# Optimization experiments

Measured on AMD Instinct MI355X. Metric: run time of the kernel, lower is better.

The kernel has to match this reference:

```python
import jax, jax.numpy as jnp
import numpy as np

B, N, F_IN, H, D = 2, 3000, 64, 4, 32
NEG = -1e9  # mask value used by the original layer

def setup_inputs() -> dict:
    key = jax.random.key(0)
    ks = jax.random.split(key, 6)
    h = jax.random.normal(ks[0], (B, N, F_IN), dtype=jnp.float32)
    # dense 0/1 adjacency
    a = jax.random.randint(ks[1], (B, N, N), 0, 2).astype(jnp.float32)
    kernel = jax.random.normal(ks[2], (H, F_IN, D), dtype=jnp.float32) * 0.1
    att_k1 = jax.random.normal(ks[3], (H, D), dtype=jnp.float32) * 0.1
    att_k2 = jax.random.normal(ks[4], (H, D), dtype=jnp.float32) * 0.1
    bias = jax.random.normal(ks[5], (H, D), dtype=jnp.float32) * 0.1
    return {"h": h, "a": a, "kernel": kernel, "att_k1": att_k1, "att_k2": att_k2, "bias": bias}

def reference(h, a, kernel, att_k1, att_k2, bias):
    # per-head projection: [B,H,N,D]
    feat = jnp.einsum('bnf,hfd->bhnd', h, kernel)
    e1 = jnp.einsum('bhnd,hd->bhn', feat, att_k1)  # attention (query part)
    e2 = jnp.einsum('bhnd,hd->bhn', feat, att_k2)  # attention_2 (key part)
    # dense branch: att = a * (e1_i + e2_j); NO LeakyReLU in dense path (faithful)
    adj = a[:, None]                                   # [B,1,N,N]
    scores = adj * (e1[..., :, None] + e2[..., None, :])
    scores = scores + jnp.where(adj == 0, jnp.float32(NEG), jnp.float32(0))
    att = jax.nn.softmax(scores, axis=-1)
    att = att * (adj != 0).astype(att.dtype)
    # dropout is identity at inference
    out = jnp.einsum('bhnm,bhmd->bhnd', att, feat)
    out = out + bias[None, :, None, :]
    out = jax.nn.relu(out)
    # zero out all-zero input nodes
    node_mask = (jnp.sum((h != 0).astype(jnp.float32), axis=-1, keepdims=True) > 0).astype(jnp.float32)  # [B,N,1]
    out = out * node_mask[:, None]
    # concat heads -> [B,N,H*D]
    return out.transpose(0, 2, 1, 3).reshape(h.shape[0], h.shape[1], -1)
```

## Files before the change

kernel.cpp:

```cpp
#include <hip/hip_runtime.h>
#include <hip/hip_bf16.h>
#include <stdint.h>

#define B_ 2
#define N_ 3000
#define F_ 64
#define H_ 4
#define D_ 32
#define K_ 128
#define KT_ 9
#define NCH_ 94
#define NROWT_ 188
#define S_ 8
#define PT_ 2304

typedef short bf16x8 __attribute__((ext_vector_type(8)));
typedef float f32x4  __attribute__((ext_vector_type(4)));

__device__ __forceinline__ unsigned short f2bf(float f) {
    uint32_t x = __float_as_uint(f);
    return (unsigned short)((x + 0x7FFFu + ((x >> 16) & 1u)) >> 16);
}

__global__ void k_feat(const float* __restrict__ hin, const float* __restrict__ kern,
                       const float* __restrict__ ak2,
                       float* __restrict__ feat, float* __restrict__ e2,
                       float* __restrict__ nmask) {
    int b = blockIdx.x / N_;
    int n = blockIdx.x % N_;
    __shared__ float hrow[F_];
    int tid = threadIdx.x;
    if (tid < F_) hrow[tid] = hin[(size_t)(b * N_ + n) * F_ + tid];
    __syncthreads();
    int hh = tid >> 5, d = tid & 31;
    float acc = 0.f;
    #pragma unroll
    for (int f = 0; f < F_; ++f)
        acc = fmaf(hrow[f], kern[(hh * F_ + f) * D_ + d], acc);
    feat[((size_t)(b * H_ + hh) * N_ + n) * D_ + d] = acc;
    float v = acc * ak2[hh * D_ + d];
    #pragma unroll
    for (int o = 16; o >= 1; o >>= 1) v += __shfl_xor(v, o, 32);
    if (d == 0) e2[(size_t)(b * H_ + hh) * N_ + n] = v;
    unsigned long long bal = __ballot(tid < F_ && hrow[tid & (F_ - 1)] != 0.0f);
    if (tid == 0) nmask[b * N_ + n] = (bal != 0ull) ? 1.0f : 0.0f;
}

__global__ void k_G(const float* __restrict__ feat, const float* __restrict__ e2,
                    bf16x8* __restrict__ G) {
    int idx = blockIdx.x * blockDim.x + threadIdx.x;
    const int total = B_ * NCH_ * KT_ * 64;
    if (idx >= total) return;
    int lane = idx & 63;
    int t  = (idx >> 6) % KT_;
    int ch = ((idx >> 6) / KT_) % NCH_;
    int b  = idx / (64 * KT_ * NCH_);
    int rg = lane >> 4, col = lane & 15;
    int k  = t * 16 + col;
    int m0 = ch * 32 + rg * 8;
    float vals[8];
    if (k < K_ + H_) {
        int hh, d; bool wonly;
        if (k < K_) { hh = k >> 5; d = k & 31; wonly = false; }
        else        { hh = k - K_; d = 0;      wonly = true;  }
        const float* e2p = e2 + (size_t)(b * H_ + hh) * N_;
        const float* fp  = feat + (size_t)(b * H_ + hh) * N_ * D_ + d;
        #pragma unroll
        for (int j = 0; j < 8; ++j) {
            int m = m0 + j;
            float v = 0.f;
            if (m < N_) {
                float w = __expf(e2p[m]);
                v = wonly ? w : w * fp[(size_t)m * D_];
            }
            vals[j] = v;
        }
    } else {
        #pragma unroll
        for (int j = 0; j < 8; ++j) vals[j] = 0.f;
    }
    union { bf16x8 v; unsigned short u[8]; } o;
    #pragma unroll
    for (int j = 0; j < 8; ++j) o.u[j] = f2bf(vals[j]);
    G[idx] = o.v;
}

__device__ __forceinline__ void loadsetA(const float* __restrict__ arow, int ch, int rg,
                                         f32x4& f0, f32x4& f1) {
    if (ch == NCH_ - 1 && rg == 3) {
        f0 = (f32x4){0.f, 0.f, 0.f, 0.f};
        f1 = (f32x4){0.f, 0.f, 0.f, 0.f};
    } else {
        const f32x4* p = (const f32x4*)(arow + ch * 32 + rg * 8);
        f0 = p[0]; f1 = p[1];
    }
}

__device__ __forceinline__ void loadsetG(const bf16x8* __restrict__ Gb, int ch,
                                         bf16x8 (&g)[KT_]) {
    const bf16x8* p = Gb + (size_t)ch * KT_ * 64;
    #pragma unroll
    for (int t = 0; t < KT_; ++t) g[t] = p[t * 64];
}

__device__ __forceinline__ void computeset(const f32x4& f0, const f32x4& f1,
                                           const bf16x8 (&g)[KT_], f32x4 (&acc)[KT_]) {
    union { uint32_t u[4]; bf16x8 v; } af;
    af.u[0] = ((f0.x != 0.f) ? 0x3F80u : 0u) | ((f0.y != 0.f) ? 0x3F800000u : 0u);
    af.u[1] = ((f0.z != 0.f) ? 0x3F80u : 0u) | ((f0.w != 0.f) ? 0x3F800000u : 0u);
    af.u[2] = ((f1.x != 0.f) ? 0x3F80u : 0u) | ((f1.y != 0.f) ? 0x3F800000u : 0u);
    af.u[3] = ((f1.z != 0.f) ? 0x3F80u : 0u) | ((f1.w != 0.f) ? 0x3F800000u : 0u);
    #pragma unroll
    for (int t = 0; t < KT_; ++t)
        acc[t] = __builtin_amdgcn_mfma_f32_16x16x32_bf16(af.v, g[t], acc[t], 0, 0, 0);
}

__global__ void __launch_bounds__(256, 2) k_main(
        const float* __restrict__ a, const bf16x8* __restrict__ G,
        float* __restrict__ partial) {
    int bid = blockIdx.x;
    int s  = bid % S_;
    int rt = (bid / S_) % NROWT_;
    int b  = bid / (S_ * NROWT_);
    int nbase = rt * 16;
    int w = threadIdx.x >> 6;
    int l = threadIdx.x & 63;
    int rg = l >> 4, col = l & 15;
    int arow_i = nbase + col;
    int aclamp = min(arow_i, N_ - 1);
    const float* arow = a + (size_t)(b * N_ + aclamp) * N_;
    const bf16x8* Gb = G + (size_t)b * NCH_ * KT_ * 64 + l;

    int g0 = (s * NCH_) / S_, g1 = ((s + 1) * NCH_) / S_;
    int len = g1 - g0;
    int c0 = g0 + (w * len) / 4;
    int c1 = g0 + ((w + 1) * len) / 4;

    f32x4 acc[KT_];
    #pragma unroll
    for (int t = 0; t < KT_; ++t) acc[t] = (f32x4){0.f, 0.f, 0.f, 0.f};

    f32x4 aA0, aA1, aB0, aB1;
    bf16x8 gA[KT_], gB[KT_];
    loadsetA(arow, c0, rg, aA0, aA1);
    loadsetG(Gb, c0, gA);
    int ch = c0;
    for (;;) {
        if (ch + 1 < c1) { loadsetA(arow, ch + 1, rg, aB0, aB1); loadsetG(Gb, ch + 1, gB); }
        computeset(aA0, aA1, gA, acc);
        if (++ch >= c1) break;
        if (ch + 1 < c1) { loadsetA(arow, ch + 1, rg, aA0, aA1); loadsetG(Gb, ch + 1, gA); }
        computeset(aB0, aB1, gB, acc);
        if (++ch >= c1) break;
    }

    __shared__ float red[4][KT_ * 4][64];
    #pragma unroll
    for (int t = 0; t < KT_; ++t)
        #pragma unroll
        for (int r = 0; r < 4; ++r)
            red[w][t * 4 + r][l] = acc[t][r];
    __syncthreads();
    float* pout = partial + (size_t)bid * PT_;
    #pragma unroll
    for (int k = 0; k < 9; ++k) {
        int flat = threadIdx.x + k * 256;
        int x = flat >> 6, y = flat & 63;
        pout[flat] = red[0][x][y] + red[1][x][y] + red[2][x][y] + red[3][x][y];
    }
}

__global__ void __launch_bounds__(256) k_red(
        const float* __restrict__ partial, const float* __restrict__ bias,
        const float* __restrict__ nmask, float* __restrict__ out) {
    int rt = blockIdx.x % NROWT_;
    int b  = blockIdx.x / NROWT_;
    int nbase = rt * 16;
    int tid = threadIdx.x;
    __shared__ float sm[PT_];
    const float* pbase = partial + (size_t)((b * NROWT_ + rt) * S_) * PT_;
    #pragma unroll
    for (int k = 0; k < 9; ++k) {
        int flat = tid + k * 256;
        float s = 0.f;
        #pragma unroll
        for (int sp = 0; sp < S_; ++sp) s += pbase[(size_t)sp * PT_ + flat];
        sm[flat] = s;
    }
    __syncthreads();
    #pragma unroll
    for (int k = 0; k < 9; ++k) {
        int flat = tid + k * 256;
        if (flat < 2048) {
            int t4r = flat >> 6;
            int t = t4r >> 2, r = t4r & 3;
            int lane = flat & 63;
            int rg = lane >> 4, col = lane & 15;
            int rowi = rg * 4 + r;
            int n = nbase + rowi;
            if (n < N_) {
                int hh = t >> 1;
                int r2 = rowi & 3, rg2 = rowi >> 2;
                float den = sm[(32 + r2) * 64 + (rg2 << 4) + hh];
                float v = (den > 0.f) ? sm[flat] / den : 0.f;
                v += bias[t * 16 + col];
                v = fmaxf(v, 0.f);
                v *= nmask[b * N_ + n];
                out[(size_t)(b * N_ + n) * K_ + t * 16 + col] = v;
            }
        }
    }
}

extern "C" void kernel_launch(void* const* d_in, const int* in_sizes, int n_in,
                              void* d_out, int out_size, void* d_ws, size_t ws_size,
                              hipStream_t stream) {
    const float* h    = (const float*)d_in[0];
    const float* a    = (const float*)d_in[1];
    const float* kern = (const float*)d_in[2];
    const float* ak2  = (const float*)d_in[4];
    const float* bias = (const float*)d_in[5];
    float* out = (float*)d_out;

    char* ws = (char*)d_ws;
    size_t o_feat  = 0;
    size_t o_e2    = o_feat  + 3072000;
    size_t o_nmask = o_e2    + 96000;
    size_t o_G     = o_nmask + 24064;
    size_t o_part  = o_G     + 1732608;
    float*  feat  = (float*)(ws + o_feat);
    float*  e2    = (float*)(ws + o_e2);
    float*  nmask = (float*)(ws + o_nmask);
    bf16x8* G     = (bf16x8*)(ws + o_G);
    float*  part  = (float*)(ws + o_part);

    k_feat<<<dim3(B_ * N_), dim3(128), 0, stream>>>(h, kern, ak2, feat, e2, nmask);
    int gtot = B_ * NCH_ * KT_ * 64;
    k_G   <<<dim3((gtot + 255) / 256), dim3(256), 0, stream>>>(feat, e2, G);
    k_main<<<dim3(B_ * NROWT_ * S_), dim3(256), 0, stream>>>(a, G, part);
    k_red <<<dim3(B_ * NROWT_), dim3(256), 0, stream>>>(part, bias, nmask, out);
}
```

Before: 53.36 us.

## Split k_main output columns across waves with LDS-staged G double buffer

Changes k_main from four waves each covering a slice of the chunk range over all nine output tiles to three waves that each cover three output tiles over the full chunk range. The G chunks are staged into shared memory via global_load_lds with double buffering and a block barrier per chunk. This removes the cross-wave LDS reduction and lowers register pressure to allow more blocks per CU. The cost is that every wave now re-reads the same adjacency row data, so A global traffic triples, and a __syncthreads is added each iteration.

```diff
diff --git a/kernel.cpp b/kernel.cpp
--- a/kernel.cpp
+++ b/kernel.cpp
@@ -13,6 +13,7 @@
 #define NROWT_ 188
 #define S_ 8
 #define PT_ 2304
+#define CHB_ 9216
 
 typedef short bf16x8 __attribute__((ext_vector_type(8)));
 typedef float f32x4  __attribute__((ext_vector_type(4)));
@@ -85,6 +86,19 @@
     G[idx] = o.v;
 }
 
+__device__ __forceinline__ void g2lds16(const void* g, void* l) {
+    __builtin_amdgcn_global_load_lds(
+        (const __attribute__((address_space(1))) void*)g,
+        (__attribute__((address_space(3))) void*)l, 16, 0, 0);
+}
+
+__device__ __forceinline__ void stage3(const char* src_ln, char* dst, int w) {
+    int c0 = 3 * w * 1024;
+    g2lds16(src_ln + c0,        dst + c0);
+    g2lds16(src_ln + c0 + 1024, dst + c0 + 1024);
+    g2lds16(src_ln + c0 + 2048, dst + c0 + 2048);
+}
+
 __device__ __forceinline__ void loadsetA(const float* __restrict__ arow, int ch, int rg,
                                          f32x4& f0, f32x4& f1) {
     if (ch == NCH_ - 1 && rg == 3) {
@@ -96,26 +110,24 @@
     }
 }
 
-__device__ __forceinline__ void loadsetG(const bf16x8* __restrict__ Gb, int ch,
-                                         bf16x8 (&g)[KT_]) {
-    const bf16x8* p = Gb + (size_t)ch * KT_ * 64;
-    #pragma unroll
-    for (int t = 0; t < KT_; ++t) g[t] = p[t * 64];
-}
-
-__device__ __forceinline__ void computeset(const f32x4& f0, const f32x4& f1,
-                                           const bf16x8 (&g)[KT_], f32x4 (&acc)[KT_]) {
+__device__ __forceinline__ void compute3(const char* gb, int loff, int tbase,
+                                         const f32x4& f0, const f32x4& f1,
+                                         f32x4 (&acc)[3]) {
     union { uint32_t u[4]; bf16x8 v; } af;
     af.u[0] = ((f0.x != 0.f) ? 0x3F80u : 0u) | ((f0.y != 0.f) ? 0x3F800000u : 0u);
     af.u[1] = ((f0.z != 0.f) ? 0x3F80u : 0u) | ((f0.w != 0.f) ? 0x3F800000u : 0u);
     af.u[2] = ((f1.x != 0.f) ? 0x3F80u : 0u) | ((f1.y != 0.f) ? 0x3F800000u : 0u);
     af.u[3] = ((f1.z != 0.f) ? 0x3F80u : 0u) | ((f1.w != 0.f) ? 0x3F800000u : 0u);
-    #pragma unroll
-    for (int t = 0; t < KT_; ++t)
-        acc[t] = __builtin_amdgcn_mfma_f32_16x16x32_bf16(af.v, g[t], acc[t], 0, 0, 0);
-}
-
-__global__ void __launch_bounds__(256, 2) k_main(
+    const char* p = gb + tbase * 1024 + loff;
+    bf16x8 g0 = *(const bf16x8*)(p);
+    bf16x8 g1 = *(const bf16x8*)(p + 1024);
+    bf16x8 g2 = *(const bf16x8*)(p + 2048);
+    acc[0] = __builtin_amdgcn_mfma_f32_16x16x32_bf16(af.v, g0, acc[0], 0, 0, 0);
+    acc[1] = __builtin_amdgcn_mfma_f32_16x16x32_bf16(af.v, g1, acc[1], 0, 0, 0);
+    acc[2] = __builtin_amdgcn_mfma_f32_16x16x32_bf16(af.v, g2, acc[2], 0, 0, 0);
+}
+
+__global__ void __launch_bounds__(192, 4) k_main(
         const float* __restrict__ a, const bf16x8* __restrict__ G,
         float* __restrict__ partial) {
     int bid = blockIdx.x;
@@ -126,47 +138,48 @@
     int w = threadIdx.x >> 6;
     int l = threadIdx.x & 63;
     int rg = l >> 4, col = l & 15;
+    int tbase = 3 * w;
     int arow_i = nbase + col;
     int aclamp = min(arow_i, N_ - 1);
     const float* arow = a + (size_t)(b * N_ + aclamp) * N_;
-    const bf16x8* Gb = G + (size_t)b * NCH_ * KT_ * 64 + l;
+    const char* Gsrc = (const char*)G + (size_t)b * NCH_ * CHB_ + (size_t)l * 16;
+
+    __shared__ __align__(16) char Gbuf[2][CHB_];
 
     int g0 = (s * NCH_) / S_, g1 = ((s + 1) * NCH_) / S_;
-    int len = g1 - g0;
-    int c0 = g0 + (w * len) / 4;
-    int c1 = g0 + ((w + 1) * len) / 4;
-
-    f32x4 acc[KT_];
-    #pragma unroll
-    for (int t = 0; t < KT_; ++t) acc[t] = (f32x4){0.f, 0.f, 0.f, 0.f};
+
+    f32x4 acc[3];
+    #pragma unroll
+    for (int i = 0; i < 3; ++i) acc[i] = (f32x4){0.f, 0.f, 0.f, 0.f};
 
     f32x4 aA0, aA1, aB0, aB1;
-    bf16x8 gA[KT_], gB[KT_];
-    loadsetA(arow, c0, rg, aA0, aA1);
-    loadsetG(Gb, c0, gA);
-    int ch = c0;
+    stage3(Gsrc + (size_t)g0 * CHB_, Gbuf[0], w);
+    loadsetA(arow, g0, rg, aA0, aA1);
+    __syncthreads();
+
+    int ch = g0, buf = 0;
     for (;;) {
-        if (ch + 1 < c1) { loadsetA(arow, ch + 1, rg, aB0, aB1); loadsetG(Gb, ch + 1, gB); }
-        computeset(aA0, aA1, gA, acc);
-        if (++ch >= c1) break;
-        if (ch + 1 < c1) { loadsetA(arow, ch + 1, rg, aA0, aA1); loadsetG(Gb, ch + 1, gA); }
-        computeset(aB0, aB1, gB, acc);
-        if (++ch >= c1) break;
-    }
-
-    __shared__ float red[4][KT_ * 4][64];
-    #pragma unroll
-    for (int t = 0; t < KT_; ++t)
+        if (ch + 1 < g1) { stage3(Gsrc + (size_t)(ch + 1) * CHB_, Gbuf[buf ^ 1], w);
+                           loadsetA(arow, ch + 1, rg, aB0, aB1); }
+        compute3(Gbuf[buf], l * 16, tbase, aA0, aA1, acc);
+        __syncthreads();
+        buf ^= 1;
+        if (++ch >= g1) break;
+        if (ch + 1 < g1) { stage3(Gsrc + (size_t)(ch + 1) * CHB_, Gbuf[buf ^ 1], w);
+                           loadsetA(arow, ch + 1, rg, aA0, aA1); }
+        compute3(Gbuf[buf], l * 16, tbase, aB0, aB1, acc);
+        __syncthreads();
+        buf ^= 1;
+        if (++ch >= g1) break;
+    }
+
+    float* pout = partial + (size_t)bid * PT_;
+    #pragma unroll
+    for (int i = 0; i < 3; ++i) {
+        int t = tbase + i;
         #pragma unroll
         for (int r = 0; r < 4; ++r)
-            red[w][t * 4 + r][l] = acc[t][r];
-    __syncthreads();
-    float* pout = partial + (size_t)bid * PT_;
-    #pragma unroll
-    for (int k = 0; k < 9; ++k) {
-        int flat = threadIdx.x + k * 256;
-        int x = flat >> 6, y = flat & 63;
-        pout[flat] = red[0][x][y] + red[1][x][y] + red[2][x][y] + red[3][x][y];
+            pout[t * 256 + r * 64 + l] = acc[i][r];
     }
 }
 
@@ -237,6 +250,6 @@
     k_feat<<<dim3(B_ * N_), dim3(128), 0, stream>>>(h, kern, ak2, feat, e2, nmask);
     int gtot = B_ * NCH_ * KT_ * 64;
     k_G   <<<dim3((gtot + 255) / 256), dim3(256), 0, stream>>>(feat, e2, G);
-    k_main<<<dim3(B_ * NROWT_ * S_), dim3(256), 0, stream>>>(a, G, part);
+    k_main<<<dim3(B_ * NROWT_ * S_), dim3(192), 0, stream>>>(a, G, part);
     k_red <<<dim3(B_ * NROWT_), dim3(256), 0, stream>>>(part, bias, nmask, out);
 }
```

After: 58.60 us. 9.8% more time.
